# Optimization experiments

Measured on AMD Instinct MI355X. Metric: run time of the kernel, lower is better.

## Reference

```python
import jax, jax.numpy as jnp
import numpy as np

H = 2048   # hidden_size
K = 2048   # key_size
Q = 2048   # query_size
S = 8192   # source sequence length
V = 2048   # value feature dim


def setup_inputs() -> dict:
    key = jax.random.key(0)
    ks = jax.random.split(key, 6)
    query = jax.random.normal(ks[0], (1, 1, Q), dtype=jnp.float32)
    src_key = jax.random.normal(ks[1], (1, S, K), dtype=jnp.float32)
    values = jax.random.normal(ks[2], (S, V), dtype=jnp.float32)
    # nn.Linear weights are [out, in]; all bias-free
    Wq = jax.random.normal(ks[3], (H, Q), dtype=jnp.float32) / np.sqrt(Q)
    Wk = jax.random.normal(ks[4], (H, K), dtype=jnp.float32) / np.sqrt(K)
    Ws = jax.random.normal(ks[5], (1, H), dtype=jnp.float32) / np.sqrt(H)
    return {"query": query, "key": src_key, "values": values,
            "Wq": Wq, "Wk": Wk, "Ws": Ws}


def reference(query, key, values, Wq, Wk, Ws):
    # projected_query: [1,1,H]; projected_key: [1,S,H]
    pq = jnp.einsum('btq,hq->bth', query, Wq)
    pk = jnp.einsum('bsk,hk->bsh', key, Wk)
    # additive (Bahdanau) scores: [1,S,1] -> squeeze(2).unsqueeze(1) -> [1,1,S]
    scores = jnp.einsum('bsh,oh->bso', jnp.tanh(pq + pk), Ws)
    scores = scores[:, :, 0][:, None, :]
    attention_weights = jax.nn.softmax(scores, axis=-1)        # [1,1,S]
    # bmm([1,1,S], values.unsqueeze(0)=[1,S,V]) -> [1,1,V]
    context = jnp.einsum('bts,sv->btv', attention_weights, values)
    return (attention_weights, context)
```

## Files before the change

kernel.cpp:

```cpp
#include <hip/hip_runtime.h>
#include <hip/hip_bf16.h>
#include <math.h>

#define HDIM 2048
#define KDIM 2048
#define SDIM 8192
#define VDIM 2048
#define BKT  64
#define NT   (KDIM / BKT)

using short8 = __attribute__((ext_vector_type(8))) short;
using f32x4  = __attribute__((ext_vector_type(4))) float;
using us8    = __attribute__((ext_vector_type(8))) unsigned short;

typedef const __attribute__((address_space(1))) void g_void;
typedef __attribute__((address_space(3))) void lds_void;

__device__ __forceinline__ unsigned short f2bf(float f) {
  union { float f; unsigned int u; } x; x.f = f;
  unsigned int r = x.u + 0x7fffu + ((x.u >> 16) & 1u);
  return (unsigned short)(r >> 16);
}

__device__ __forceinline__ float tanh_fast(float x) {
  float e = __expf(2.0f * x);
  return 1.0f - 2.0f * __builtin_amdgcn_rcpf(e + 1.0f);
}

__device__ __forceinline__ void barrier_sync() {
  asm volatile("" ::: "memory");
  __builtin_amdgcn_s_barrier();
  asm volatile("" ::: "memory");
}

__global__ __launch_bounds__(256) void cvt_pq_kernel(const float* __restrict__ key,
                                                     const float* __restrict__ Wk,
                                                     unsigned short* __restrict__ outbf,
                                                     const float* __restrict__ query,
                                                     const float* __restrict__ Wq,
                                                     float* __restrict__ pq,
                                                     int keyN8, int cvtBlocks) {
  if ((int)blockIdx.x < cvtBlocks) {
    int i = blockIdx.x * 256 + threadIdx.x;
    const float* src = (i < keyN8) ? &key[(size_t)i * 8] : &Wk[((size_t)i - keyN8) * 8];
    f32x4 a = __builtin_nontemporal_load((const f32x4*)src);
    f32x4 b = __builtin_nontemporal_load((const f32x4*)(src + 4));
    us8 o;
    #pragma unroll
    for (int j = 0; j < 4; ++j) { o[j] = f2bf(a[j]); o[j + 4] = f2bf(b[j]); }
    *(us8*)&outbf[(size_t)i * 8] = o;
  } else {
    int wave = threadIdx.x >> 6, lane = threadIdx.x & 63;
    int h = (blockIdx.x - cvtBlocks) * 4 + wave;
    const float* w = Wq + (size_t)h * KDIM;
    f32x4 s4 = (f32x4)(0.0f);
    #pragma unroll
    for (int i = 0; i < KDIM / 256; ++i) {
      f32x4 q4 = *(const f32x4*)&query[lane * 4 + i * 256];
      f32x4 w4 = __builtin_nontemporal_load((const f32x4*)&w[lane * 4 + i * 256]);
      #pragma unroll
      for (int j = 0; j < 4; ++j) s4[j] = fmaf(q4[j], w4[j], s4[j]);
    }
    float s = s4[0] + s4[1] + s4[2] + s4[3];
    #pragma unroll
    for (int off = 32; off; off >>= 1) s += __shfl_xor(s, off);
    if (lane == 0) pq[h] = s;
  }
}

__global__ __launch_bounds__(512, 2) void scores_kernel(const unsigned short* __restrict__ keybf,
                                                        const unsigned short* __restrict__ wkbf,
                                                        const float* __restrict__ pq,
                                                        const float* __restrict__ Ws,
                                                        float* __restrict__ partial) {
  __shared__ unsigned short lds[65536];

  const int tid = threadIdx.x;
  const int bid = blockIdx.x;
  const int xg = bid & 7, xi = bid >> 3;
  const int bx = xg * 4 + (xi & 3);
  const int by = xi >> 2;
  const int s0 = bx * 256, h0 = by * 256;

  const int wave = tid >> 6, lane = tid & 63;
  const int wm = wave >> 2, wn = wave & 3;
  const int l16 = lane & 15, g16 = lane >> 4;

  const int srow = tid >> 3;
  const int scol = ((tid & 7) * 16) ^ ((srow & 7) << 4);
  const char* aSrc0 = (const char*)keybf + ((size_t)(s0 + srow) * KDIM) * 2 + scol;
  const char* bSrc0 = (const char*)wkbf  + ((size_t)(h0 + srow) * KDIM) * 2 + scol;

  #define STAGE_A(o, kt, buf) __builtin_amdgcn_global_load_lds( \
      (g_void*)(aSrc0 + (size_t)(o) * 64 * KDIM * 2 + (size_t)(kt) * 128), \
      (lds_void*)((char*)lds + (size_t)(buf) * 65536 + (o) * 8192 + wave * 1024), 16, 0, 0)
  #define STAGE_B(o, kt, buf) __builtin_amdgcn_global_load_lds( \
      (g_void*)(bSrc0 + (size_t)(o) * 64 * KDIM * 2 + (size_t)(kt) * 128), \
      (lds_void*)((char*)lds + (size_t)(buf) * 65536 + 32768 + (o) * 8192 + wave * 1024), 16, 0, 0)

  const int xorv = (l16 & 7) << 4;
  int colx[2];
  colx[0] = ((g16 * 16)      ) ^ xorv;
  colx[1] = ((g16 * 16) | 64 ) ^ xorv;
  const int aRowBase = (wm * 128 + l16) * 128;
  const int bRowBase = 32768 + (wn * 64 + l16) * 128;

  f32x4 acc[8][4];
  #pragma unroll
  for (int m = 0; m < 8; ++m)
    #pragma unroll
    for (int n = 0; n < 4; ++n) acc[m][n] = (f32x4)(0.0f);

  STAGE_A(0, 0, 0); STAGE_A(1, 0, 0); STAGE_A(2, 0, 0); STAGE_A(3, 0, 0);
  STAGE_B(0, 0, 0); STAGE_B(1, 0, 0); STAGE_B(2, 0, 0); STAGE_B(3, 0, 0);
  asm volatile("s_waitcnt vmcnt(0)" ::: "memory");
  barrier_sync();

  short8 af[4][2], bf_[4][2];

  for (int t = 0; t < NT; ++t) {
    const int cbase = (t & 1) * 65536;
    const int nbuf = (t & 1) ^ 1;
    const bool more = (t + 1 < NT);

    #pragma unroll
    for (int m = 0; m < 4; ++m)
      #pragma unroll
      for (int ks = 0; ks < 2; ++ks)
        af[m][ks] = *(const short8*)((const char*)lds + cbase + aRowBase + m * 2048 + colx[ks]);
    #pragma unroll
    for (int n = 0; n < 4; ++n)
      #pragma unroll
      for (int ks = 0; ks < 2; ++ks)
        bf_[n][ks] = *(const short8*)((const char*)lds + cbase + bRowBase + n * 2048 + colx[ks]);

    if (more) {
      STAGE_A(0, t + 1, nbuf); STAGE_A(1, t + 1, nbuf);
      STAGE_A(2, t + 1, nbuf); STAGE_A(3, t + 1, nbuf);
      STAGE_B(0, t + 1, nbuf); STAGE_B(1, t + 1, nbuf);
      STAGE_B(2, t + 1, nbuf); STAGE_B(3, t + 1, nbuf);
    }

    __builtin_amdgcn_s_setprio(1);
    #pragma unroll
    for (int ks = 0; ks < 2; ++ks)
      #pragma unroll
      for (int m = 0; m < 4; ++m)
        #pragma unroll
        for (int n = 0; n < 4; ++n)
          acc[m][n] = __builtin_amdgcn_mfma_f32_16x16x32_bf16(af[m][ks], bf_[n][ks], acc[m][n], 0, 0, 0);
    __builtin_amdgcn_s_setprio(0);

    #pragma unroll
    for (int m = 0; m < 4; ++m)
      #pragma unroll
      for (int ks = 0; ks < 2; ++ks)
        af[m][ks] = *(const short8*)((const char*)lds + cbase + aRowBase + (m + 4) * 2048 + colx[ks]);

    __builtin_amdgcn_s_setprio(1);
    #pragma unroll
    for (int ks = 0; ks < 2; ++ks)
      #pragma unroll
      for (int m = 0; m < 4; ++m)
        #pragma unroll
        for (int n = 0; n < 4; ++n)
          acc[m + 4][n] = __builtin_amdgcn_mfma_f32_16x16x32_bf16(af[m][ks], bf_[n][ks], acc[m + 4][n], 0, 0, 0);
    __builtin_amdgcn_s_setprio(0);

    asm volatile("s_waitcnt vmcnt(0)" ::: "memory");
    barrier_sync();
  }

  float pqv[4], wsv[4];
  #pragma unroll
  for (int n = 0; n < 4; ++n) {
    int h = h0 + wn * 64 + n * 16 + l16;
    pqv[n] = pq[h];
    wsv[n] = Ws[h];
  }

  float* sred = (float*)lds;
  #pragma unroll
  for (int m = 0; m < 8; ++m) {
    #pragma unroll
    for (int j = 0; j < 4; ++j) {
      float rs = 0.f;
      #pragma unroll
      for (int n = 0; n < 4; ++n)
        rs += tanh_fast(acc[m][n][j] + pqv[n]) * wsv[n];
      rs += __shfl_xor(rs, 1);
      rs += __shfl_xor(rs, 2);
      rs += __shfl_xor(rs, 4);
      rs += __shfl_xor(rs, 8);
      if (l16 == 0)
        sred[(wm * 128 + m * 16 + g16 * 4 + j) * 4 + wn] = rs;
    }
  }
  __syncthreads();
  if (tid < 256) {
    float v = sred[tid * 4 + 0] + sred[tid * 4 + 1] + sred[tid * 4 + 2] + sred[tid * 4 + 3];
    partial[(size_t)(s0 + tid) * 8 + by] = v;
  }
}

__global__ __launch_bounds__(256) void smax_part_kernel(const float* __restrict__ partial,
                                                        float* __restrict__ wexp,
                                                        float* __restrict__ pairs) {
  __shared__ float red[8];
  int tid = threadIdx.x, wave = tid >> 6, lane = tid & 63;
  int s = blockIdx.x * 256 + tid;
  const float* p = partial + (size_t)s * 8;
  float v = 0.f;
  #pragma unroll
  for (int q = 0; q < 8; ++q) v += p[q];
  float mx = v;
  #pragma unroll
  for (int off = 32; off; off >>= 1) mx = fmaxf(mx, __shfl_xor(mx, off));
  if (lane == 0) red[wave] = mx;
  __syncthreads();
  float bmax = fmaxf(fmaxf(red[0], red[1]), fmaxf(red[2], red[3]));
  float e = __expf(v - bmax);
  wexp[s] = e;
  float sm = e;
  #pragma unroll
  for (int off = 32; off; off >>= 1) sm += __shfl_xor(sm, off);
  if (lane == 0) red[4 + wave] = sm;
  __syncthreads();
  if (tid == 0)
    { pairs[blockIdx.x * 2] = bmax; pairs[blockIdx.x * 2 + 1] = red[4] + red[5] + red[6] + red[7]; }
}

__global__ __launch_bounds__(256) void ctx_fused_kernel(const float* __restrict__ values,
                                                        const float* __restrict__ wexp,
                                                        const float* __restrict__ pairs,
                                                        float* __restrict__ weights,
                                                        float* __restrict__ ctx) {
  __shared__ float scl[32];
  __shared__ f32x4 sred[256];
  int tid = threadIdx.x, b = blockIdx.x;

  float gmax = -1e30f;
  #pragma unroll
  for (int i = 0; i < 32; ++i) gmax = fmaxf(gmax, pairs[2 * i]);
  float gs = 0.f;
  #pragma unroll
  for (int i = 0; i < 32; ++i) gs += pairs[2 * i + 1] * __expf(pairs[2 * i] - gmax);
  if (tid < 32) scl[tid] = __expf(pairs[2 * tid] - gmax);
  __syncthreads();
  float inv = 1.0f / gs;

  if (b < 32) {
    int s = b * 256 + tid;
    weights[s] = wexp[s] * scl[b] * inv;
  }

  const int c4 = b * 2 + (tid & 1);
  const int g  = tid >> 1;
  f32x4 acc = (f32x4)(0.0f);
  for (int s = g; s < SDIM; s += 128) {
    float w = wexp[s] * scl[s >> 8];
    f32x4 v = *(const f32x4*)&values[(size_t)s * VDIM + c4 * 4];
    #pragma unroll
    for (int j = 0; j < 4; ++j) acc[j] = fmaf(w, v[j], acc[j]);
  }
  sred[tid] = acc;
  #pragma unroll
  for (int step = 64; step; step >>= 1) {
    __syncthreads();
    if (g < step) {
      f32x4 a = sred[tid], o = sred[tid + step * 2];
      #pragma unroll
      for (int j = 0; j < 4; ++j) a[j] += o[j];
      sred[tid] = a;
    }
  }
  __syncthreads();
  if (tid < 2) {
    f32x4 a = sred[tid];
    #pragma unroll
    for (int j = 0; j < 4; ++j) a[j] *= inv;
    *(f32x4*)&ctx[(size_t)(b * 2 + tid) * 4] = a;
  }
}

extern "C" void kernel_launch(void* const* d_in, const int* in_sizes, int n_in,
                              void* d_out, int out_size, void* d_ws, size_t ws_size,
                              hipStream_t stream) {
  const float* query  = (const float*)d_in[0];
  const float* key    = (const float*)d_in[1];
  const float* values = (const float*)d_in[2];
  const float* Wq     = (const float*)d_in[3];
  const float* Wk     = (const float*)d_in[4];
  const float* Ws     = (const float*)d_in[5];

  float* out     = (float*)d_out;
  float* weights = out;
  float* ctx     = out + SDIM;

  char* ws = (char*)d_ws;
  unsigned short* keybf = (unsigned short*)ws;
  unsigned short* wkbf  = (unsigned short*)(ws + (size_t)SDIM * KDIM * 2);
  char* tail = ws + (size_t)SDIM * KDIM * 2 + (size_t)HDIM * KDIM * 2;
  float* pq      = (float*)tail;
  float* partial = (float*)(tail + 8192);
  float* wexp    = (float*)(tail + 8192 + (size_t)SDIM * 8 * 4);
  float* pairs   = wexp + SDIM;

  const int keyN8 = SDIM * KDIM / 8;
  const int totN8 = keyN8 + HDIM * KDIM / 8;
  const int cvtBlocks = totN8 / 256;
  cvt_pq_kernel<<<cvtBlocks + HDIM / 4, 256, 0, stream>>>(key, Wk, keybf, query, Wq, pq,
                                                          keyN8, cvtBlocks);
  scores_kernel<<<256, 512, 0, stream>>>(keybf, wkbf, pq, Ws, partial);
  smax_part_kernel<<<32, 256, 0, stream>>>(partial, wexp, pairs);
  ctx_fused_kernel<<<256, 256, 0, stream>>>(values, wexp, pairs, weights, ctx);
}
```

Measured before the change: 126.6 us.

## Switch scores GEMM to 32x32 MFMA and fold softmax into context kernel

The scores GEMM now uses 32x32x16 bf16 MFMA tiles instead of 16x16x32. The LDS read addressing, accumulator layout and the tanh/Ws epilogue reduction are remapped to match. The separate softmax-partial kernel is removed: every context block recomputes the full-row max and sum of exp from the partial scores, keeping all 8192 weights in LDS. This drops one launch and the wexp/pairs round trip through global memory. In exchange, each of the 256 blocks does redundant softmax work and uses 32KB of LDS, which may reduce occupancy.

```diff
diff --git a/kernel.cpp b/kernel.cpp
--- a/kernel.cpp
+++ b/kernel.cpp
@@ -11,6 +11,7 @@
 
 using short8 = __attribute__((ext_vector_type(8))) short;
 using f32x4  = __attribute__((ext_vector_type(4))) float;
+using f32x16 = __attribute__((ext_vector_type(16))) float;
 using us8    = __attribute__((ext_vector_type(8))) unsigned short;
 
 typedef const __attribute__((address_space(1))) void g_void;
@@ -84,7 +85,7 @@
 
   const int wave = tid >> 6, lane = tid & 63;
   const int wm = wave >> 2, wn = wave & 3;
-  const int l16 = lane & 15, g16 = lane >> 4;
+  const int l31 = lane & 31, hi5 = lane >> 5, l7 = lane & 7;
 
   const int srow = tid >> 3;
   const int scol = ((tid & 7) * 16) ^ ((srow & 7) << 4);
@@ -98,25 +99,25 @@
       (g_void*)(bSrc0 + (size_t)(o) * 64 * KDIM * 2 + (size_t)(kt) * 128), \
       (lds_void*)((char*)lds + (size_t)(buf) * 65536 + 32768 + (o) * 8192 + wave * 1024), 16, 0, 0)
 
-  const int xorv = (l16 & 7) << 4;
-  int colx[2];
-  colx[0] = ((g16 * 16)      ) ^ xorv;
-  colx[1] = ((g16 * 16) | 64 ) ^ xorv;
-  const int aRowBase = (wm * 128 + l16) * 128;
-  const int bRowBase = 32768 + (wn * 64 + l16) * 128;
-
-  f32x4 acc[8][4];
-  #pragma unroll
-  for (int m = 0; m < 8; ++m)
-    #pragma unroll
-    for (int n = 0; n < 4; ++n) acc[m][n] = (f32x4)(0.0f);
+  int cread[4];
+  #pragma unroll
+  for (int ks = 0; ks < 4; ++ks)
+    cread[ks] = (((ks * 2 + hi5) ^ l7) << 4);
+  const int aBase = (wm * 128 + l31) * 128;
+  const int bBase = 32768 + (wn * 64 + l31) * 128;
+
+  f32x16 acc[4][2];
+  #pragma unroll
+  for (int m = 0; m < 4; ++m)
+    #pragma unroll
+    for (int n = 0; n < 2; ++n) acc[m][n] = (f32x16)(0.0f);
 
   STAGE_A(0, 0, 0); STAGE_A(1, 0, 0); STAGE_A(2, 0, 0); STAGE_A(3, 0, 0);
   STAGE_B(0, 0, 0); STAGE_B(1, 0, 0); STAGE_B(2, 0, 0); STAGE_B(3, 0, 0);
   asm volatile("s_waitcnt vmcnt(0)" ::: "memory");
   barrier_sync();
 
-  short8 af[4][2], bf_[4][2];
+  short8 af[4][2], bf_[2][2];
 
   for (int t = 0; t < NT; ++t) {
     const int cbase = (t & 1) * 65536;
@@ -124,15 +125,15 @@
     const bool more = (t + 1 < NT);
 
     #pragma unroll
-    for (int m = 0; m < 4; ++m)
+    for (int mt = 0; mt < 4; ++mt)
       #pragma unroll
       for (int ks = 0; ks < 2; ++ks)
-        af[m][ks] = *(const short8*)((const char*)lds + cbase + aRowBase + m * 2048 + colx[ks]);
-    #pragma unroll
-    for (int n = 0; n < 4; ++n)
+        af[mt][ks] = *(const short8*)((const char*)lds + cbase + aBase + mt * 4096 + cread[ks]);
+    #pragma unroll
+    for (int nt = 0; nt < 2; ++nt)
       #pragma unroll
       for (int ks = 0; ks < 2; ++ks)
-        bf_[n][ks] = *(const short8*)((const char*)lds + cbase + bRowBase + n * 2048 + colx[ks]);
+        bf_[nt][ks] = *(const short8*)((const char*)lds + cbase + bBase + nt * 4096 + cread[ks]);
 
     if (more) {
       STAGE_A(0, t + 1, nbuf); STAGE_A(1, t + 1, nbuf);
@@ -145,55 +146,59 @@
     #pragma unroll
     for (int ks = 0; ks < 2; ++ks)
       #pragma unroll
-      for (int m = 0; m < 4; ++m)
+      for (int mt = 0; mt < 4; ++mt)
         #pragma unroll
-        for (int n = 0; n < 4; ++n)
-          acc[m][n] = __builtin_amdgcn_mfma_f32_16x16x32_bf16(af[m][ks], bf_[n][ks], acc[m][n], 0, 0, 0);
+        for (int nt = 0; nt < 2; ++nt)
+          acc[mt][nt] = __builtin_amdgcn_mfma_f32_32x32x16_bf16(af[mt][ks], bf_[nt][ks], acc[mt][nt], 0, 0, 0);
     __builtin_amdgcn_s_setprio(0);
 
     #pragma unroll
-    for (int m = 0; m < 4; ++m)
+    for (int mt = 0; mt < 4; ++mt)
       #pragma unroll
       for (int ks = 0; ks < 2; ++ks)
-        af[m][ks] = *(const short8*)((const char*)lds + cbase + aRowBase + (m + 4) * 2048 + colx[ks]);
+        af[mt][ks] = *(const short8*)((const char*)lds + cbase + aBase + mt * 4096 + cread[ks + 2]);
+    #pragma unroll
+    for (int nt = 0; nt < 2; ++nt)
+      #pragma unroll
+      for (int ks = 0; ks < 2; ++ks)
+        bf_[nt][ks] = *(const short8*)((const char*)lds + cbase + bBase + nt * 4096 + cread[ks + 2]);
 
     __builtin_amdgcn_s_setprio(1);
     #pragma unroll
     for (int ks = 0; ks < 2; ++ks)
       #pragma unroll
-      for (int m = 0; m < 4; ++m)
+      for (int mt = 0; mt < 4; ++mt)
         #pragma unroll
-        for (int n = 0; n < 4; ++n)
-          acc[m + 4][n] = __builtin_amdgcn_mfma_f32_16x16x32_bf16(af[m][ks], bf_[n][ks], acc[m + 4][n], 0, 0, 0);
+        for (int nt = 0; nt < 2; ++nt)
+          acc[mt][nt] = __builtin_amdgcn_mfma_f32_32x32x16_bf16(af[mt][ks], bf_[nt][ks], acc[mt][nt], 0, 0, 0);
     __builtin_amdgcn_s_setprio(0);
 
     asm volatile("s_waitcnt vmcnt(0)" ::: "memory");
     barrier_sync();
   }
 
-  float pqv[4], wsv[4];
-  #pragma unroll
-  for (int n = 0; n < 4; ++n) {
-    int h = h0 + wn * 64 + n * 16 + l16;
-    pqv[n] = pq[h];
-    wsv[n] = Ws[h];
+  float pqv[2], wsv[2];
+  #pragma unroll
+  for (int nt = 0; nt < 2; ++nt) {
+    int h = h0 + wn * 64 + nt * 32 + l31;
+    pqv[nt] = pq[h];
+    wsv[nt] = Ws[h];
   }
 
   float* sred = (float*)lds;
   #pragma unroll
-  for (int m = 0; m < 8; ++m) {
-    #pragma unroll
-    for (int j = 0; j < 4; ++j) {
-      float rs = 0.f;
-      #pragma unroll
-      for (int n = 0; n < 4; ++n)
-        rs += tanh_fast(acc[m][n][j] + pqv[n]) * wsv[n];
+  for (int mt = 0; mt < 4; ++mt) {
+    #pragma unroll
+    for (int reg = 0; reg < 16; ++reg) {
+      float rs = tanh_fast(acc[mt][0][reg] + pqv[0]) * wsv[0]
+               + tanh_fast(acc[mt][1][reg] + pqv[1]) * wsv[1];
       rs += __shfl_xor(rs, 1);
       rs += __shfl_xor(rs, 2);
       rs += __shfl_xor(rs, 4);
       rs += __shfl_xor(rs, 8);
-      if (l16 == 0)
-        sred[(wm * 128 + m * 16 + g16 * 4 + j) * 4 + wn] = rs;
+      rs += __shfl_xor(rs, 16);
+      if (l31 == 0)
+        sred[(wm * 128 + mt * 32 + (reg & 3) + 8 * (reg >> 2) + 4 * hi5) * 4 + wn] = rs;
     }
   }
   __syncthreads();
@@ -203,62 +208,53 @@
   }
 }
 
-__global__ __launch_bounds__(256) void smax_part_kernel(const float* __restrict__ partial,
-                                                        float* __restrict__ wexp,
-                                                        float* __restrict__ pairs) {
-  __shared__ float red[8];
-  int tid = threadIdx.x, wave = tid >> 6, lane = tid & 63;
-  int s = blockIdx.x * 256 + tid;
-  const float* p = partial + (size_t)s * 8;
-  float v = 0.f;
-  #pragma unroll
-  for (int q = 0; q < 8; ++q) v += p[q];
-  float mx = v;
-  #pragma unroll
-  for (int off = 32; off; off >>= 1) mx = fmaxf(mx, __shfl_xor(mx, off));
-  if (lane == 0) red[wave] = mx;
-  __syncthreads();
-  float bmax = fmaxf(fmaxf(red[0], red[1]), fmaxf(red[2], red[3]));
-  float e = __expf(v - bmax);
-  wexp[s] = e;
-  float sm = e;
-  #pragma unroll
-  for (int off = 32; off; off >>= 1) sm += __shfl_xor(sm, off);
-  if (lane == 0) red[4 + wave] = sm;
-  __syncthreads();
-  if (tid == 0)
-    { pairs[blockIdx.x * 2] = bmax; pairs[blockIdx.x * 2 + 1] = red[4] + red[5] + red[6] + red[7]; }
-}
-
 __global__ __launch_bounds__(256) void ctx_fused_kernel(const float* __restrict__ values,
-                                                        const float* __restrict__ wexp,
-                                                        const float* __restrict__ pairs,
+                                                        const float* __restrict__ partial,
                                                         float* __restrict__ weights,
                                                         float* __restrict__ ctx) {
-  __shared__ float scl[32];
+  __shared__ float wls[SDIM];
+  __shared__ float red[8];
   __shared__ f32x4 sred[256];
   int tid = threadIdx.x, b = blockIdx.x;
-
-  float gmax = -1e30f;
-  #pragma unroll
-  for (int i = 0; i < 32; ++i) gmax = fmaxf(gmax, pairs[2 * i]);
-  float gs = 0.f;
-  #pragma unroll
-  for (int i = 0; i < 32; ++i) gs += pairs[2 * i + 1] * __expf(pairs[2 * i] - gmax);
-  if (tid < 32) scl[tid] = __expf(pairs[2 * tid] - gmax);
+  int lane = tid & 63, wave = tid >> 6;
+
+  float lmax = -1e30f;
+  for (int r = tid; r < SDIM; r += 256) {
+    const float* p = partial + (size_t)r * 8;
+    f32x4 x0 = *(const f32x4*)p, x1 = *(const f32x4*)(p + 4);
+    float v = x0[0] + x0[1] + x0[2] + x0[3] + x1[0] + x1[1] + x1[2] + x1[3];
+    wls[r] = v;
+    lmax = fmaxf(lmax, v);
+  }
+  #pragma unroll
+  for (int off = 32; off; off >>= 1) lmax = fmaxf(lmax, __shfl_xor(lmax, off));
+  if (lane == 0) red[wave] = lmax;
   __syncthreads();
+  float gmax = fmaxf(fmaxf(red[0], red[1]), fmaxf(red[2], red[3]));
+
+  float lsum = 0.f;
+  for (int r = tid; r < SDIM; r += 256) {
+    float e = __expf(wls[r] - gmax);
+    wls[r] = e;
+    lsum += e;
+  }
+  #pragma unroll
+  for (int off = 32; off; off >>= 1) lsum += __shfl_xor(lsum, off);
+  if (lane == 0) red[4 + wave] = lsum;
+  __syncthreads();
+  float gs = red[4] + red[5] + red[6] + red[7];
   float inv = 1.0f / gs;
 
   if (b < 32) {
     int s = b * 256 + tid;
-    weights[s] = wexp[s] * scl[b] * inv;
+    weights[s] = wls[s] * inv;
   }
 
   const int c4 = b * 2 + (tid & 1);
   const int g  = tid >> 1;
   f32x4 acc = (f32x4)(0.0f);
   for (int s = g; s < SDIM; s += 128) {
-    float w = wexp[s] * scl[s >> 8];
+    float w = wls[s];
     f32x4 v = *(const f32x4*)&values[(size_t)s * VDIM + c4 * 4];
     #pragma unroll
     for (int j = 0; j < 4; ++j) acc[j] = fmaf(w, v[j], acc[j]);
@@ -303,8 +299,6 @@
   char* tail = ws + (size_t)SDIM * KDIM * 2 + (size_t)HDIM * KDIM * 2;
   float* pq      = (float*)tail;
   float* partial = (float*)(tail + 8192);
-  float* wexp    = (float*)(tail + 8192 + (size_t)SDIM * 8 * 4);
-  float* pairs   = wexp + SDIM;
 
   const int keyN8 = SDIM * KDIM / 8;
   const int totN8 = keyN8 + HDIM * KDIM / 8;
@@ -312,6 +306,5 @@
   cvt_pq_kernel<<<cvtBlocks + HDIM / 4, 256, 0, stream>>>(key, Wk, keybf, query, Wq, pq,
                                                           keyN8, cvtBlocks);
   scores_kernel<<<256, 512, 0, stream>>>(keybf, wkbf, pq, Ws, partial);
-  smax_part_kernel<<<32, 256, 0, stream>>>(partial, wexp, pairs);
-  ctx_fused_kernel<<<256, 256, 0, stream>>>(values, wexp, pairs, weights, ctx);
-}
+  ctx_fused_kernel<<<256, 256, 0, stream>>>(values, partial, weights, ctx);
+}
```

Result: slower. 149.8 us (+18.3%).
